# Kernel optimization log

Hardware: AMD Instinct MI355X
Metric: run time of the kernel (lower is better)

Reference implementation:

```python
import jax, jax.numpy as jnp
import numpy as np

B, S, D, H = 2, 2048, 1024, 16
DK = D // H

def setup_inputs() -> dict:
    key = jax.random.key(0)
    ks = jax.random.split(key, 12)
    scale = 1.0 / np.sqrt(D)
    inp = {
        'q': jax.random.normal(ks[0], (B, S, D), jnp.float32),
        'k': jax.random.normal(ks[1], (B, S, D), jnp.float32),
        'v': jax.random.normal(ks[2], (B, S, D), jnp.float32),
        # causal mask: 1 where attending is allowed (j <= i), 0 for future tokens
        'mask': jnp.tril(jnp.ones((S, S), jnp.int32))[None, None, :, :],
        'wq': jax.random.normal(ks[3], (D, D), jnp.float32) * scale,
        'bq': jnp.zeros((D,), jnp.float32),
        'wk': jax.random.normal(ks[4], (D, D), jnp.float32) * scale,
        'bk': jnp.zeros((D,), jnp.float32),
        'wv': jax.random.normal(ks[5], (D, D), jnp.float32) * scale,
        'bv': jnp.zeros((D,), jnp.float32),
        'wo': jax.random.normal(ks[6], (D, D), jnp.float32) * scale,
        'bo': jnp.zeros((D,), jnp.float32),
    }
    return inp


def reference(q, k, v, mask, wq, bq, wk, bk, wv, bv, wo, bo):
    def split_heads(x):
        # [B,S,D] -> [B,H,S,DK]
        return x.reshape(B, S, H, DK).transpose(0, 2, 1, 3)

    query = split_heads(q @ wq + bq)
    key_ = split_heads(k @ wk + bk)
    value = split_heads(v @ wv + bv)

    # [B,H,S,S] attention scores
    scores = jnp.einsum('bhqd,bhkd->bhqk', query, key_) / jnp.sqrt(
        jnp.asarray(DK, jnp.float32))
    scores = jnp.where(mask == 0, jnp.asarray(-1e9, scores.dtype), scores)
    attn = jax.nn.softmax(scores, axis=-1)  # dropout p=0.0 (eval mode)

    x = jnp.einsum('bhqk,bhkd->bhqd', attn, value)  # [B,H,S,DK]
    x = x.transpose(0, 2, 1, 3).reshape(B, S, D)
    return x @ wo + bo
```

## Files before the change

kernel.cpp:

```cpp
#include <hip/hip_runtime.h>
#include <hip/hip_bf16.h>

#define BATCH 2
#define SEQ   2048
#define DMODEL 1024
#define NHEAD 16
#define DK    64
#define MTOK  (BATCH * SEQ)

typedef __attribute__((ext_vector_type(8))) short bf16x8;
typedef __attribute__((ext_vector_type(4))) float f32x4;

__device__ __forceinline__ unsigned short f2bf(float x) {
    unsigned u = __float_as_uint(x);
    u = (u + 0x7FFFu + ((u >> 16) & 1u)) >> 16;
    return (unsigned short)u;
}

__device__ __forceinline__ void store_out(float* p, float v)          { *p = v; }
__device__ __forceinline__ void store_out(unsigned short* p, float v) { *p = f2bf(v); }

__device__ __forceinline__ unsigned cvt_pk_bf16(float x, float y) {
    unsigned d;
    asm("v_cvt_pk_bf16_f32 %0, %1, %2" : "=v"(d) : "v"(x), "v"(y));
    return d;
}

__device__ __forceinline__ void g2lds16(const void* g, void* l) {
    __builtin_amdgcn_global_load_lds(
        (const __attribute__((address_space(1))) void*)g,
        (__attribute__((address_space(3))) void*)l, 16, 0, 0);
}

template <int N>
__device__ __forceinline__ void s_wait_vmcnt() {
    asm volatile("s_waitcnt vmcnt(%0)" :: "n"(N) : "memory");
}
__device__ __forceinline__ void s_wait_lgkm0() {
    asm volatile("s_waitcnt lgkmcnt(0)" ::: "memory");
}
__device__ __forceinline__ void s_bar() {
    asm volatile("s_barrier" ::: "memory");
}

__global__ __launch_bounds__(256) void cvtw_kernel(
    const float* __restrict__ q, const float* __restrict__ k,
    const float* __restrict__ v,
    unsigned short* __restrict__ dq, unsigned short* __restrict__ dk,
    unsigned short* __restrict__ dv,
    const float* __restrict__ w0, const float* __restrict__ w1,
    const float* __restrict__ w2, const float* __restrict__ w3,
    unsigned short* __restrict__ t0, unsigned short* __restrict__ t1,
    unsigned short* __restrict__ t2, unsigned short* __restrict__ t3, int n)
{
    __shared__ float tile[32][33];
    if (blockIdx.z < 3) {
        const float* src; unsigned short* dst;
        switch (blockIdx.z) {
            case 0:  src = q; dst = dq; break;
            case 1:  src = k; dst = dk; break;
            default: src = v; dst = dv; break;
        }
        int i = (blockIdx.x * 256 + threadIdx.x) * 8;
        if (i >= n) return;
        float4 a = *(const float4*)(src + i);
        float4 b = *(const float4*)(src + i + 4);
        union { unsigned short s[8]; uint4 u; } o;
        o.s[0] = f2bf(a.x); o.s[1] = f2bf(a.y); o.s[2] = f2bf(a.z); o.s[3] = f2bf(a.w);
        o.s[4] = f2bf(b.x); o.s[5] = f2bf(b.y); o.s[6] = f2bf(b.z); o.s[7] = f2bf(b.w);
        *(uint4*)(dst + i) = o.u;
    } else {
        const int wi = (blockIdx.z - 3) * 2 + (blockIdx.x >> 10);
        const float* W; unsigned short* T;
        switch (wi) {
            case 0:  W = w0; T = t0; break;
            case 1:  W = w1; T = t1; break;
            case 2:  W = w2; T = t2; break;
            default: W = w3; T = t3; break;
        }
        const int ti = blockIdx.x & 1023;
        const int n0 = (ti & 31) * 32, k0 = (ti >> 5) * 32;
        const int t  = threadIdx.x;
        const int r  = t >> 3;
        const int c4 = (t & 7) * 4;

        float4 vv = *(const float4*)&W[(size_t)(k0 + r) * DMODEL + n0 + c4];
        tile[r][c4 + 0] = vv.x; tile[r][c4 + 1] = vv.y;
        tile[r][c4 + 2] = vv.z; tile[r][c4 + 3] = vv.w;
        __syncthreads();

        union { unsigned short s[4]; uint2 u; } o;
#pragma unroll
        for (int u = 0; u < 4; ++u) o.s[u] = f2bf(tile[c4 + u][r]);
        *(uint2*)&T[(size_t)(n0 + r) * DMODEL + k0 + c4] = o.u;
    }
}

struct GemmP {
    const unsigned short* A;
    const unsigned short* Bt;
    const float* bias;
    void* C;
    int N, K, ctShift, biasByRow;
    float scale;
};
struct Gemm3 { GemmP p[3]; };

template <typename OutT, int MR, int NC, bool SPLITK>
__device__ __forceinline__ void gemm_body(const Gemm3& g)
{
    constexpr int AM    = MR / 2;
    constexpr int NCW   = NC / 4;
    constexpr int NBLK  = 2 * MR + 2 * NC;
    constexpr int PW    = NBLK / 8;
    constexpr int BUFSZ = NBLK * 512;

    __shared__ unsigned short sS[2 * BUFSZ];

    const unsigned nx  = gridDim.x;
    const unsigned lin = blockIdx.x + nx * blockIdx.z;
    const unsigned ch  = (nx * gridDim.z) >> 3;
    const unsigned l2  = (lin & 7u) * ch + (lin >> 3);
    const unsigned zz  = l2 / nx;
    const unsigned bid0 = l2 - zz * nx;

    const GemmP p = g.p[zz];
    const unsigned short* __restrict__ A  = p.A;
    const unsigned short* __restrict__ Bt = p.Bt;
    OutT* __restrict__ C = (OutT*)p.C;
    const int K = p.K, N = p.N;

    int ks = 0; unsigned bid = bid0;
    if constexpr (SPLITK) { ks = (int)(bid0 >> 8); bid = bid0 & 255u; }
    const int kbase = SPLITK ? ks * (K >> 1) : 0;
    const int KS    = SPLITK ? (K >> 1) : K;

    const int bx = (int)(bid & ((1u << p.ctShift) - 1u));
    const int by = (int)(bid >> p.ctShift);
    const int row0 = by * (MR * 16);
    const int col0 = bx * (NC * 16);

    const int t    = threadIdx.x;
    const int w    = t >> 6;
    const int lane = t & 63;
    const int ln   = lane & 15;
    const int qg   = lane >> 4;
    const int wm   = w >> 2;
    const int wn   = w & 3;

    const unsigned short* sp[PW];
    int lo[PW];
#pragma unroll
    for (int i = 0; i < PW; ++i) {
        const int s = w * PW + i;
        if (s < 2 * MR) {
            const int mtg = s >> 1, kc = s & 1;
            sp[i] = A + (size_t)(row0 + mtg * 16 + ln) * K + kbase + kc * 32 + qg * 8;
        } else {
            const int bi = s - 2 * MR;
            const int ntg = bi >> 1, kc = bi & 1;
            sp[i] = Bt + (size_t)(col0 + ntg * 16 + ln) * K + kbase + kc * 32 + qg * 8;
        }
        lo[i] = s * 512;
    }

    f32x4 acc[AM][NCW];
#pragma unroll
    for (int mt = 0; mt < AM; ++mt)
#pragma unroll
        for (int nt = 0; nt < NCW; ++nt) acc[mt][nt] = (f32x4){0.f, 0.f, 0.f, 0.f};

    const int NT = KS / 64;

#pragma unroll
    for (int i = 0; i < PW; ++i) g2lds16(sp[i], &sS[lo[i]]);
#pragma unroll
    for (int i = 0; i < PW; ++i) g2lds16(sp[i] + 64, &sS[BUFSZ + lo[i]]);

    int curOff = 0;
    for (int kt = 0; kt < NT; ++kt) {
        if (kt < NT - 1) s_wait_vmcnt<PW>();
        else             s_wait_vmcnt<0>();
        s_bar();

        const unsigned short* bufA = &sS[curOff];
        const unsigned short* bufB = &sS[curOff + 2 * MR * 512];
#pragma unroll
        for (int kc = 0; kc < 2; ++kc) {
            bf16x8 aF[AM], bF[NCW];
#pragma unroll
            for (int mt = 0; mt < AM; ++mt)
                aF[mt] = *(const bf16x8*)&bufA[(((wm * AM + mt) * 2) + kc) * 512 + lane * 8];
#pragma unroll
            for (int n2 = 0; n2 < NCW; ++n2)
                bF[n2] = *(const bf16x8*)&bufB[(((wn * NCW + n2) * 2) + kc) * 512 + lane * 8];
#pragma unroll
            for (int mt = 0; mt < AM; ++mt)
#pragma unroll
                for (int n2 = 0; n2 < NCW; ++n2)
                    acc[mt][n2] = __builtin_amdgcn_mfma_f32_16x16x32_bf16(
                        aF[mt], bF[n2], acc[mt][n2], 0, 0, 0);
        }

        s_wait_lgkm0();
        s_bar();

        if (kt + 2 < NT) {
            const int koff = (kt + 2) * 64;
#pragma unroll
            for (int i = 0; i < PW; ++i)
                g2lds16(sp[i] + koff, &sS[curOff + lo[i]]);
        }
        curOff ^= BUFSZ;
    }

    float bcol[NCW], brow[AM][4];
    if (!p.biasByRow) {
#pragma unroll
        for (int n2 = 0; n2 < NCW; ++n2)
            bcol[n2] = p.bias[col0 + (wn * NCW + n2) * 16 + ln];
    } else {
#pragma unroll
        for (int mt = 0; mt < AM; ++mt)
#pragma unroll
            for (int r = 0; r < 4; ++r)
                brow[mt][r] = p.bias[row0 + wm * (AM * 16) + mt * 16 + qg * 4 + r];
    }
    const bool addBias = !SPLITK || (ks == 0);

#pragma unroll
    for (int mt = 0; mt < AM; ++mt)
#pragma unroll
        for (int n2 = 0; n2 < NCW; ++n2)
#pragma unroll
            for (int r = 0; r < 4; ++r) {
                int row = row0 + wm * (AM * 16) + mt * 16 + qg * 4 + r;
                int col = col0 + (wn * NCW + n2) * 16 + ln;
                float bb = p.biasByRow ? brow[mt][r] : bcol[n2];
                float vv = (acc[mt][n2][r] + (addBias ? bb : 0.f)) * p.scale;
                if constexpr (SPLITK) atomicAdd((float*)&C[(size_t)row * N + col], vv);
                else                  store_out(&C[(size_t)row * N + col], vv);
            }
}

__global__ __launch_bounds__(512, 2) void gemm_qkv_kernel(Gemm3 g)
{
    gemm_body<unsigned short, 16, 16, false>(g);
}
__global__ __launch_bounds__(512, 2) void gemm_out_kernel(Gemm3 g)
{
    gemm_body<float, 8, 8, true>(g);
}

#define BR 64
#define BC 64

__global__ __launch_bounds__(256) void attn_mfma_kernel(
    const unsigned short* __restrict__ Qg, const unsigned short* __restrict__ Kg,
    const unsigned short* __restrict__ VT, unsigned short* __restrict__ O)
{
    __shared__ unsigned short sK[2][8 * 512];
    __shared__ unsigned short sV[2][8 * 512];
    __shared__ unsigned short sQ[8 * 512];

    const int t    = threadIdx.x;
    const int w    = t >> 6;
    const int lane = t & 63;
    const int ln   = lane & 15;
    const int qg   = lane >> 4;

    const int id  = blockIdx.x;
    const int bh  = id & 31;
    const int qt  = (SEQ / BR - 1) - (id >> 5);
    const int b   = bh >> 4;
    const int h   = bh & 15;
    const int qi0 = qt * BR;

    const size_t rowbase = (size_t)b * SEQ;
    const size_t colbase = (size_t)h * DK;

#pragma unroll
    for (int i = 0; i < 2; ++i) {
        const int s = w * 2 + i;
        const int nt = s >> 1, kc = s & 1;
        g2lds16(Qg + (rowbase + qi0 + w * 16 + ln) * DMODEL + colbase + i * 32 + qg * 8,
                &sQ[s * 512]);
        g2lds16(Kg + (rowbase + nt * 16 + ln) * DMODEL + colbase + kc * 32 + qg * 8,
                &sK[0][s * 512]);
        g2lds16(VT + (size_t)(colbase + nt * 16 + ln) * MTOK + rowbase + kc * 32 + qg * 8,
                &sV[0][s * 512]);
    }
    __syncthreads();

    bf16x8 aq[2];
#pragma unroll
    for (int kc = 0; kc < 2; ++kc)
        aq[kc] = *(const bf16x8*)&sQ[(w * 2 + kc) * 512 + lane * 8];

    f32x4 ofrag[4];
#pragma unroll
    for (int nt = 0; nt < 4; ++nt) ofrag[nt] = (f32x4){0.f, 0.f, 0.f, 0.f};
    float osum_p = 0.f;
    float m_run  = -3.0e38f;

    const int laneA = ((2 * qg) & 3) * 16 + ln;
    const int laneB = ((2 * qg + 1) & 3) * 16 + ln;
    const bool hiSel = (qg >> 1) & 1;

    const int ntiles = qt + 1;
    for (int jt = 0; jt < ntiles; ++jt) {
        const int cur = jt & 1;

        if (jt + 1 < ntiles) {
            const int j1 = (jt + 1) * BC;
            const int nb = cur ^ 1;
#pragma unroll
            for (int i = 0; i < 2; ++i) {
                const int s = w * 2 + i;
                const int nt = s >> 1, kc = s & 1;
                g2lds16(Kg + (rowbase + j1 + nt * 16 + ln) * DMODEL + colbase + kc * 32 + qg * 8,
                        &sK[nb][s * 512]);
                g2lds16(VT + (size_t)(colbase + nt * 16 + ln) * MTOK + rowbase + j1 + kc * 32 + qg * 8,
                        &sV[nb][s * 512]);
            }
        }

        f32x4 sf[4];
#pragma unroll
        for (int nt = 0; nt < 4; ++nt) {
            f32x4 a2 = (f32x4){0.f, 0.f, 0.f, 0.f};
#pragma unroll
            for (int kc = 0; kc < 2; ++kc) {
                bf16x8 bk = *(const bf16x8*)&sK[cur][(nt * 2 + kc) * 512 + lane * 8];
                a2 = __builtin_amdgcn_mfma_f32_16x16x32_bf16(bk, aq[kc], a2, 0, 0, 0);
            }
            sf[nt] = a2;
        }

        if (jt == ntiles - 1) {
            const int qloc = w * 16 + ln;
#pragma unroll
            for (int nt = 0; nt < 4; ++nt)
#pragma unroll
                for (int r = 0; r < 4; ++r)
                    if (nt * 16 + qg * 4 + r > qloc) sf[nt][r] = -1.0e30f;
        }

        float pmax = sf[0][0];
#pragma unroll
        for (int nt = 0; nt < 4; ++nt)
#pragma unroll
            for (int r = 0; r < 4; ++r) pmax = fmaxf(pmax, sf[nt][r]);
        pmax = fmaxf(pmax, __shfl_xor(pmax, 16));
        pmax = fmaxf(pmax, __shfl_xor(pmax, 32));

        const float mn = fmaxf(m_run, pmax);
        const float al = exp2f(m_run - mn);
        m_run = mn;

        float pv[4][4];
        float lsum = 0.f;
#pragma unroll
        for (int nt = 0; nt < 4; ++nt)
#pragma unroll
            for (int r = 0; r < 4; ++r) {
                float e = exp2f(sf[nt][r] - mn);
                pv[nt][r] = e;
                lsum += e;
            }
        osum_p = osum_p * al + lsum;

        float alr[4];
#pragma unroll
        for (int r = 0; r < 4; ++r) alr[r] = __shfl(al, qg * 4 + r);
#pragma unroll
        for (int nt = 0; nt < 4; ++nt)
#pragma unroll
            for (int r = 0; r < 4; ++r) ofrag[nt][r] *= alr[r];

        unsigned pk0[2], pk1[2], pk2[2], pk3[2];
#pragma unroll
        for (int rr = 0; rr < 2; ++rr) {
            pk0[rr] = cvt_pk_bf16(pv[0][2 * rr], pv[0][2 * rr + 1]);
            pk1[rr] = cvt_pk_bf16(pv[1][2 * rr], pv[1][2 * rr + 1]);
            pk2[rr] = cvt_pk_bf16(pv[2][2 * rr], pv[2][2 * rr + 1]);
            pk3[rr] = cvt_pk_bf16(pv[3][2 * rr], pv[3][2 * rr + 1]);
        }
        union { bf16x8 v; unsigned u[4]; } ap[2];
        {
            unsigned s0, s1;
            s0 = (unsigned)__shfl((int)pk0[0], laneA); s1 = (unsigned)__shfl((int)pk1[0], laneA);
            ap[0].u[0] = hiSel ? s1 : s0;
            s0 = (unsigned)__shfl((int)pk0[1], laneA); s1 = (unsigned)__shfl((int)pk1[1], laneA);
            ap[0].u[1] = hiSel ? s1 : s0;
            s0 = (unsigned)__shfl((int)pk0[0], laneB); s1 = (unsigned)__shfl((int)pk1[0], laneB);
            ap[0].u[2] = hiSel ? s1 : s0;
            s0 = (unsigned)__shfl((int)pk0[1], laneB); s1 = (unsigned)__shfl((int)pk1[1], laneB);
            ap[0].u[3] = hiSel ? s1 : s0;
            s0 = (unsigned)__shfl((int)pk2[0], laneA); s1 = (unsigned)__shfl((int)pk3[0], laneA);
            ap[1].u[0] = hiSel ? s1 : s0;
            s0 = (unsigned)__shfl((int)pk2[1], laneA); s1 = (unsigned)__shfl((int)pk3[1], laneA);
            ap[1].u[1] = hiSel ? s1 : s0;
            s0 = (unsigned)__shfl((int)pk2[0], laneB); s1 = (unsigned)__shfl((int)pk3[0], laneB);
            ap[1].u[2] = hiSel ? s1 : s0;
            s0 = (unsigned)__shfl((int)pk2[1], laneB); s1 = (unsigned)__shfl((int)pk3[1], laneB);
            ap[1].u[3] = hiSel ? s1 : s0;
        }

#pragma unroll
        for (int nt = 0; nt < 4; ++nt) {
#pragma unroll
            for (int kc = 0; kc < 2; ++kc) {
                bf16x8 bv = *(const bf16x8*)&sV[cur][(nt * 2 + kc) * 512 + lane * 8];
                ofrag[nt] = __builtin_amdgcn_mfma_f32_16x16x32_bf16(ap[kc].v, bv, ofrag[nt], 0, 0, 0);
            }
        }

        __syncthreads();
    }

    float osum = osum_p + __shfl_xor(osum_p, 16);
    osum += __shfl_xor(osum, 32);
    const float invq = 1.0f / osum;
    float inv[4];
#pragma unroll
    for (int r = 0; r < 4; ++r) inv[r] = __shfl(invq, qg * 4 + r);
#pragma unroll
    for (int nt = 0; nt < 4; ++nt)
#pragma unroll
        for (int r = 0; r < 4; ++r) {
            int gq = qi0 + w * 16 + qg * 4 + r;
            O[(rowbase + gq) * DMODEL + colbase + nt * 16 + ln] =
                f2bf(ofrag[nt][r] * inv[r]);
        }
}

extern "C" void kernel_launch(void* const* d_in, const int* in_sizes, int n_in,
                              void* d_out, int out_size, void* d_ws, size_t ws_size,
                              hipStream_t stream)
{
    const float* q  = (const float*)d_in[0];
    const float* k  = (const float*)d_in[1];
    const float* v  = (const float*)d_in[2];
    const float* wq = (const float*)d_in[4];
    const float* bq = (const float*)d_in[5];
    const float* wk = (const float*)d_in[6];
    const float* bk = (const float*)d_in[7];
    const float* wv = (const float*)d_in[8];
    const float* bv = (const float*)d_in[9];
    const float* wo = (const float*)d_in[10];
    const float* bo = (const float*)d_in[11];
    float* out = (float*)d_out;

    const size_t mat  = (size_t)MTOK * DMODEL;
    const size_t wmat = (size_t)DMODEL * DMODEL;
    unsigned short* Abq = (unsigned short*)d_ws;
    unsigned short* Abk = Abq + mat;
    unsigned short* Abv = Abk + mat;
    unsigned short* WtQ = Abv + mat;
    unsigned short* WtK = WtQ + wmat;
    unsigned short* WtV = WtK + wmat;
    unsigned short* WtO = WtV + wmat;
    unsigned short* Qb  = WtO + wmat;
    unsigned short* Kb  = Qb + mat;
    unsigned short* VT  = Kb + mat;
    unsigned short* CTX = VT + mat;

    hipMemsetAsync(out, 0, mat * sizeof(float), stream);

    cvtw_kernel<<<dim3(2048, 1, 5), 256, 0, stream>>>(
        q, k, v, Abq, Abk, Abv, wq, wk, wv, wo, WtQ, WtK, WtV, WtO, (int)mat);

    const float qscale = 0.125f * 1.44269504088896f;
    Gemm3 g;
    g.p[0] = (GemmP){Abq, WtQ, bq, (void*)Qb, DMODEL, DMODEL, 2, 0, qscale};
    g.p[1] = (GemmP){Abk, WtK, bk, (void*)Kb, DMODEL, DMODEL, 2, 0, 1.0f};
    g.p[2] = (GemmP){WtV, Abv, bv, (void*)VT, MTOK,   DMODEL, 4, 1, 1.0f};
    gemm_qkv_kernel<<<dim3(64, 1, 3), 512, 0, stream>>>(g);

    attn_mfma_kernel<<<BATCH * NHEAD * (SEQ / BR), 256, 0, stream>>>(Qb, Kb, VT, CTX);

    Gemm3 go;
    go.p[0] = (GemmP){CTX, WtO, bo, (void*)out, DMODEL, DMODEL, 3, 0, 1.0f};
    go.p[1] = go.p[0];
    go.p[2] = go.p[0];
    gemm_out_kernel<<<dim3(512, 1, 1), 512, 0, stream>>>(go);
}
```

Measured before the change: 279.7 us.

## Enlarge attention query tile to 128 rows and drop split-K in output GEMM

The attention kernel now processes 128 query rows per block with 8 waves, so each K/V tile loaded into shared memory is reused by twice as many queries. Each wave now loads one slice of the K/V tiles instead of two, and the causal masking is generalised to cover the last two key tiles. The output projection GEMM no longer splits K in two with atomic adds, which also removes the memset of the output buffer. In exchange there are half as many attention blocks with more imbalanced causal work, and fewer output GEMM blocks with longer K loops.

```diff
diff --git a/kernel.cpp b/kernel.cpp
--- a/kernel.cpp
+++ b/kernel.cpp
@@ -106,7 +106,7 @@
 };
 struct Gemm3 { GemmP p[3]; };
 
-template <typename OutT, int MR, int NC, bool SPLITK>
+template <typename OutT, int MR, int NC>
 __device__ __forceinline__ void gemm_body(const Gemm3& g)
 {
     constexpr int AM    = MR / 2;
@@ -122,18 +122,13 @@
     const unsigned ch  = (nx * gridDim.z) >> 3;
     const unsigned l2  = (lin & 7u) * ch + (lin >> 3);
     const unsigned zz  = l2 / nx;
-    const unsigned bid0 = l2 - zz * nx;
+    const unsigned bid = l2 - zz * nx;
 
     const GemmP p = g.p[zz];
     const unsigned short* __restrict__ A  = p.A;
     const unsigned short* __restrict__ Bt = p.Bt;
     OutT* __restrict__ C = (OutT*)p.C;
     const int K = p.K, N = p.N;
-
-    int ks = 0; unsigned bid = bid0;
-    if constexpr (SPLITK) { ks = (int)(bid0 >> 8); bid = bid0 & 255u; }
-    const int kbase = SPLITK ? ks * (K >> 1) : 0;
-    const int KS    = SPLITK ? (K >> 1) : K;
 
     const int bx = (int)(bid & ((1u << p.ctShift) - 1u));
     const int by = (int)(bid >> p.ctShift);
@@ -155,11 +150,11 @@
         const int s = w * PW + i;
         if (s < 2 * MR) {
             const int mtg = s >> 1, kc = s & 1;
-            sp[i] = A + (size_t)(row0 + mtg * 16 + ln) * K + kbase + kc * 32 + qg * 8;
+            sp[i] = A + (size_t)(row0 + mtg * 16 + ln) * K + kc * 32 + qg * 8;
         } else {
             const int bi = s - 2 * MR;
             const int ntg = bi >> 1, kc = bi & 1;
-            sp[i] = Bt + (size_t)(col0 + ntg * 16 + ln) * K + kbase + kc * 32 + qg * 8;
+            sp[i] = Bt + (size_t)(col0 + ntg * 16 + ln) * K + kc * 32 + qg * 8;
         }
         lo[i] = s * 512;
     }
@@ -170,7 +165,7 @@
 #pragma unroll
         for (int nt = 0; nt < NCW; ++nt) acc[mt][nt] = (f32x4){0.f, 0.f, 0.f, 0.f};
 
-    const int NT = KS / 64;
+    const int NT = K / 64;
 
 #pragma unroll
     for (int i = 0; i < PW; ++i) g2lds16(sp[i], &sS[lo[i]]);
@@ -226,7 +221,6 @@
             for (int r = 0; r < 4; ++r)
                 brow[mt][r] = p.bias[row0 + wm * (AM * 16) + mt * 16 + qg * 4 + r];
     }
-    const bool addBias = !SPLITK || (ks == 0);
 
 #pragma unroll
     for (int mt = 0; mt < AM; ++mt)
@@ -237,31 +231,29 @@
                 int row = row0 + wm * (AM * 16) + mt * 16 + qg * 4 + r;
                 int col = col0 + (wn * NCW + n2) * 16 + ln;
                 float bb = p.biasByRow ? brow[mt][r] : bcol[n2];
-                float vv = (acc[mt][n2][r] + (addBias ? bb : 0.f)) * p.scale;
-                if constexpr (SPLITK) atomicAdd((float*)&C[(size_t)row * N + col], vv);
-                else                  store_out(&C[(size_t)row * N + col], vv);
+                store_out(&C[(size_t)row * N + col], (acc[mt][n2][r] + bb) * p.scale);
             }
 }
 
 __global__ __launch_bounds__(512, 2) void gemm_qkv_kernel(Gemm3 g)
 {
-    gemm_body<unsigned short, 16, 16, false>(g);
+    gemm_body<unsigned short, 16, 16>(g);
 }
 __global__ __launch_bounds__(512, 2) void gemm_out_kernel(Gemm3 g)
 {
-    gemm_body<float, 8, 8, true>(g);
-}
-
-#define BR 64
+    gemm_body<float, 8, 8>(g);
+}
+
+#define BR 128
 #define BC 64
 
-__global__ __launch_bounds__(256) void attn_mfma_kernel(
+__global__ __launch_bounds__(512) void attn_mfma_kernel(
     const unsigned short* __restrict__ Qg, const unsigned short* __restrict__ Kg,
     const unsigned short* __restrict__ VT, unsigned short* __restrict__ O)
 {
     __shared__ unsigned short sK[2][8 * 512];
     __shared__ unsigned short sV[2][8 * 512];
-    __shared__ unsigned short sQ[8 * 512];
+    __shared__ unsigned short sQ[16 * 512];
 
     const int t    = threadIdx.x;
     const int w    = t >> 6;
@@ -279,17 +271,18 @@
     const size_t rowbase = (size_t)b * SEQ;
     const size_t colbase = (size_t)h * DK;
 
+    const int snt = w >> 1, skc = w & 1;
+
 #pragma unroll
     for (int i = 0; i < 2; ++i) {
         const int s = w * 2 + i;
-        const int nt = s >> 1, kc = s & 1;
         g2lds16(Qg + (rowbase + qi0 + w * 16 + ln) * DMODEL + colbase + i * 32 + qg * 8,
                 &sQ[s * 512]);
-        g2lds16(Kg + (rowbase + nt * 16 + ln) * DMODEL + colbase + kc * 32 + qg * 8,
-                &sK[0][s * 512]);
-        g2lds16(VT + (size_t)(colbase + nt * 16 + ln) * MTOK + rowbase + kc * 32 + qg * 8,
-                &sV[0][s * 512]);
-    }
+    }
+    g2lds16(Kg + (rowbase + snt * 16 + ln) * DMODEL + colbase + skc * 32 + qg * 8,
+            &sK[0][w * 512]);
+    g2lds16(VT + (size_t)(colbase + snt * 16 + ln) * MTOK + rowbase + skc * 32 + qg * 8,
+            &sV[0][w * 512]);
     __syncthreads();
 
     bf16x8 aq[2];
@@ -307,22 +300,17 @@
     const int laneB = ((2 * qg + 1) & 3) * 16 + ln;
     const bool hiSel = (qg >> 1) & 1;
 
-    const int ntiles = qt + 1;
+    const int ntiles = 2 * qt + 2;
     for (int jt = 0; jt < ntiles; ++jt) {
         const int cur = jt & 1;
 
         if (jt + 1 < ntiles) {
             const int j1 = (jt + 1) * BC;
             const int nb = cur ^ 1;
-#pragma unroll
-            for (int i = 0; i < 2; ++i) {
-                const int s = w * 2 + i;
-                const int nt = s >> 1, kc = s & 1;
-                g2lds16(Kg + (rowbase + j1 + nt * 16 + ln) * DMODEL + colbase + kc * 32 + qg * 8,
-                        &sK[nb][s * 512]);
-                g2lds16(VT + (size_t)(colbase + nt * 16 + ln) * MTOK + rowbase + j1 + kc * 32 + qg * 8,
-                        &sV[nb][s * 512]);
-            }
+            g2lds16(Kg + (rowbase + j1 + snt * 16 + ln) * DMODEL + colbase + skc * 32 + qg * 8,
+                    &sK[nb][w * 512]);
+            g2lds16(VT + (size_t)(colbase + snt * 16 + ln) * MTOK + rowbase + j1 + skc * 32 + qg * 8,
+                    &sV[nb][w * 512]);
         }
 
         f32x4 sf[4];
@@ -337,13 +325,14 @@
             sf[nt] = a2;
         }
 
-        if (jt == ntiles - 1) {
-            const int qloc = w * 16 + ln;
+        if (jt >= ntiles - 2) {
+            const int qglob = qi0 + w * 16 + ln;
+            const int kb = jt * BC;
 #pragma unroll
             for (int nt = 0; nt < 4; ++nt)
 #pragma unroll
                 for (int r = 0; r < 4; ++r)
-                    if (nt * 16 + qg * 4 + r > qloc) sf[nt][r] = -1.0e30f;
+                    if (kb + nt * 16 + qg * 4 + r > qglob) sf[nt][r] = -1.0e30f;
         }
 
         float pmax = sf[0][0];
@@ -466,8 +455,6 @@
     unsigned short* VT  = Kb + mat;
     unsigned short* CTX = VT + mat;
 
-    hipMemsetAsync(out, 0, mat * sizeof(float), stream);
-
     cvtw_kernel<<<dim3(2048, 1, 5), 256, 0, stream>>>(
         q, k, v, Abq, Abk, Abv, wq, wk, wv, wo, WtQ, WtK, WtV, WtO, (int)mat);
 
@@ -478,11 +465,11 @@
     g.p[2] = (GemmP){WtV, Abv, bv, (void*)VT, MTOK,   DMODEL, 4, 1, 1.0f};
     gemm_qkv_kernel<<<dim3(64, 1, 3), 512, 0, stream>>>(g);
 
-    attn_mfma_kernel<<<BATCH * NHEAD * (SEQ / BR), 256, 0, stream>>>(Qb, Kb, VT, CTX);
+    attn_mfma_kernel<<<BATCH * NHEAD * (SEQ / BR), 512, 0, stream>>>(Qb, Kb, VT, CTX);
 
     Gemm3 go;
     go.p[0] = (GemmP){CTX, WtO, bo, (void*)out, DMODEL, DMODEL, 3, 0, 1.0f};
     go.p[1] = go.p[0];
     go.p[2] = go.p[0];
-    gemm_out_kernel<<<dim3(512, 1, 1), 512, 0, stream>>>(go);
-}
+    gemm_out_kernel<<<dim3(256, 1, 1), 512, 0, stream>>>(go);
+}
```

After: 262.1 us. 1.07x faster.

## Drop split-K atomics in output GEMM and add lazy softmax rescaling

Applied to the files above, without the earlier changes.

The output projection no longer splits K across two blocks with atomicAdd into a zeroed buffer. Each of 256 blocks now computes the full K range and stores directly, which removes the memset and the atomic traffic but halves the parallelism of that launch. In attention, the running max and the rescaling of the output accumulator are updated only when some row's new tile max exceeds the running max by more than 8 (in log2 units). Otherwise the stale max is kept, which skips the shuffles and multiplies but lets exponentials reach up to 2^8 before normalisation.

```diff
diff --git a/kernel.cpp b/kernel.cpp
--- a/kernel.cpp
+++ b/kernel.cpp
@@ -106,7 +106,7 @@
 };
 struct Gemm3 { GemmP p[3]; };
 
-template <typename OutT, int MR, int NC, bool SPLITK>
+template <typename OutT, int MR, int NC>
 __device__ __forceinline__ void gemm_body(const Gemm3& g)
 {
     constexpr int AM    = MR / 2;
@@ -122,18 +122,13 @@
     const unsigned ch  = (nx * gridDim.z) >> 3;
     const unsigned l2  = (lin & 7u) * ch + (lin >> 3);
     const unsigned zz  = l2 / nx;
-    const unsigned bid0 = l2 - zz * nx;
+    const unsigned bid = l2 - zz * nx;
 
     const GemmP p = g.p[zz];
     const unsigned short* __restrict__ A  = p.A;
     const unsigned short* __restrict__ Bt = p.Bt;
     OutT* __restrict__ C = (OutT*)p.C;
     const int K = p.K, N = p.N;
-
-    int ks = 0; unsigned bid = bid0;
-    if constexpr (SPLITK) { ks = (int)(bid0 >> 8); bid = bid0 & 255u; }
-    const int kbase = SPLITK ? ks * (K >> 1) : 0;
-    const int KS    = SPLITK ? (K >> 1) : K;
 
     const int bx = (int)(bid & ((1u << p.ctShift) - 1u));
     const int by = (int)(bid >> p.ctShift);
@@ -155,11 +150,11 @@
         const int s = w * PW + i;
         if (s < 2 * MR) {
             const int mtg = s >> 1, kc = s & 1;
-            sp[i] = A + (size_t)(row0 + mtg * 16 + ln) * K + kbase + kc * 32 + qg * 8;
+            sp[i] = A + (size_t)(row0 + mtg * 16 + ln) * K + kc * 32 + qg * 8;
         } else {
             const int bi = s - 2 * MR;
             const int ntg = bi >> 1, kc = bi & 1;
-            sp[i] = Bt + (size_t)(col0 + ntg * 16 + ln) * K + kbase + kc * 32 + qg * 8;
+            sp[i] = Bt + (size_t)(col0 + ntg * 16 + ln) * K + kc * 32 + qg * 8;
         }
         lo[i] = s * 512;
     }
@@ -170,7 +165,7 @@
 #pragma unroll
         for (int nt = 0; nt < NCW; ++nt) acc[mt][nt] = (f32x4){0.f, 0.f, 0.f, 0.f};
 
-    const int NT = KS / 64;
+    const int NT = K / 64;
 
 #pragma unroll
     for (int i = 0; i < PW; ++i) g2lds16(sp[i], &sS[lo[i]]);
@@ -226,7 +221,6 @@
             for (int r = 0; r < 4; ++r)
                 brow[mt][r] = p.bias[row0 + wm * (AM * 16) + mt * 16 + qg * 4 + r];
     }
-    const bool addBias = !SPLITK || (ks == 0);
 
 #pragma unroll
     for (int mt = 0; mt < AM; ++mt)
@@ -237,19 +231,17 @@
                 int row = row0 + wm * (AM * 16) + mt * 16 + qg * 4 + r;
                 int col = col0 + (wn * NCW + n2) * 16 + ln;
                 float bb = p.biasByRow ? brow[mt][r] : bcol[n2];
-                float vv = (acc[mt][n2][r] + (addBias ? bb : 0.f)) * p.scale;
-                if constexpr (SPLITK) atomicAdd((float*)&C[(size_t)row * N + col], vv);
-                else                  store_out(&C[(size_t)row * N + col], vv);
+                store_out(&C[(size_t)row * N + col], (acc[mt][n2][r] + bb) * p.scale);
             }
 }
 
 __global__ __launch_bounds__(512, 2) void gemm_qkv_kernel(Gemm3 g)
 {
-    gemm_body<unsigned short, 16, 16, false>(g);
+    gemm_body<unsigned short, 16, 16>(g);
 }
 __global__ __launch_bounds__(512, 2) void gemm_out_kernel(Gemm3 g)
 {
-    gemm_body<float, 8, 8, true>(g);
+    gemm_body<float, 8, 8>(g);
 }
 
 #define BR 64
@@ -354,9 +346,19 @@
         pmax = fmaxf(pmax, __shfl_xor(pmax, 16));
         pmax = fmaxf(pmax, __shfl_xor(pmax, 32));
 
-        const float mn = fmaxf(m_run, pmax);
-        const float al = exp2f(m_run - mn);
-        m_run = mn;
+        if (!__all(pmax - m_run <= 8.0f)) {
+            const float mn = fmaxf(m_run, pmax);
+            const float al = exp2f(m_run - mn);
+            m_run = mn;
+            float alr[4];
+#pragma unroll
+            for (int r = 0; r < 4; ++r) alr[r] = __shfl(al, qg * 4 + r);
+#pragma unroll
+            for (int nt = 0; nt < 4; ++nt)
+#pragma unroll
+                for (int r = 0; r < 4; ++r) ofrag[nt][r] *= alr[r];
+            osum_p *= al;
+        }
 
         float pv[4][4];
         float lsum = 0.f;
@@ -364,19 +366,11 @@
         for (int nt = 0; nt < 4; ++nt)
 #pragma unroll
             for (int r = 0; r < 4; ++r) {
-                float e = exp2f(sf[nt][r] - mn);
+                float e = exp2f(sf[nt][r] - m_run);
                 pv[nt][r] = e;
                 lsum += e;
             }
-        osum_p = osum_p * al + lsum;
-
-        float alr[4];
-#pragma unroll
-        for (int r = 0; r < 4; ++r) alr[r] = __shfl(al, qg * 4 + r);
-#pragma unroll
-        for (int nt = 0; nt < 4; ++nt)
-#pragma unroll
-            for (int r = 0; r < 4; ++r) ofrag[nt][r] *= alr[r];
+        osum_p += lsum;
 
         unsigned pk0[2], pk1[2], pk2[2], pk3[2];
 #pragma unroll
@@ -466,8 +460,6 @@
     unsigned short* VT  = Kb + mat;
     unsigned short* CTX = VT + mat;
 
-    hipMemsetAsync(out, 0, mat * sizeof(float), stream);
-
     cvtw_kernel<<<dim3(2048, 1, 5), 256, 0, stream>>>(
         q, k, v, Abq, Abk, Abv, wq, wk, wv, wo, WtQ, WtK, WtV, WtO, (int)mat);
 
@@ -484,5 +476,5 @@
     go.p[0] = (GemmP){CTX, WtO, bo, (void*)out, DMODEL, DMODEL, 3, 0, 1.0f};
     go.p[1] = go.p[0];
     go.p[2] = go.p[0];
-    gemm_out_kernel<<<dim3(512, 1, 1), 512, 0, stream>>>(go);
-}
+    gemm_out_kernel<<<dim3(256, 1, 1), 512, 0, stream>>>(go);
+}
```

Result: faster. 252.7 us (-9.6%).
